# Kernel tuning notes

Hardware: AMD Instinct MI355X
Metric: run time of the kernel (lower is better)

Reference implementation:

```python
import jax, jax.numpy as jnp
import numpy as np

EMBED_DIM = 256; NUM_HEADS = 8; NUM_LEVELS = 4; NUM_POINTS = 4; FFN_DIM = 1024
SHAPES = [(128, 128), (64, 64), (32, 32), (16, 16)]
LN_EPS = 1e-5


def setup_inputs() -> dict:
    key = jax.random.key(0)
    ks = jax.random.split(key, 12)
    B = 2; C = EMBED_DIM
    Lin = sum(h * w for h, w in SHAPES)
    starts = np.concatenate([[0], np.cumsum([h * w for h, w in SHAPES])[:-1]])
    MLP2 = NUM_HEADS * NUM_LEVELS * NUM_POINTS
    p = lambda k, *s: jax.random.normal(k, s, jnp.float32) * 0.05
    return {
        "src": jax.random.normal(ks[0], (B, Lin, C), jnp.float32),
        "pos": jax.random.normal(ks[1], (B, Lin, C), jnp.float32),
        "reference_points": jax.random.uniform(ks[2], (B, Lin, NUM_LEVELS, 2), jnp.float32),
        "Wv": p(ks[3], C, C), "bv": jnp.zeros((C,), jnp.float32),
        "Wo": p(ks[4], C, MLP2 * 2),
        "bo": jax.random.uniform(ks[5], (MLP2 * 2,), jnp.float32, -2.0, 2.0),
        "Wa": p(ks[6], C, MLP2), "ba": jnp.zeros((MLP2,), jnp.float32),
        "Wout": p(ks[7], C, C), "bout": jnp.zeros((C,), jnp.float32),
        "gamma": jnp.ones((C,), jnp.float32), "beta": jnp.zeros((C,), jnp.float32),
        "W1": p(ks[8], C, FFN_DIM), "b1": jnp.zeros((FFN_DIM,), jnp.float32),
        "W2": p(ks[9], FFN_DIM, C), "b2": jnp.zeros((C,), jnp.float32),
        "spatial_shapes": jnp.array(SHAPES, dtype=jnp.int32),
        "level_start_index": jnp.array(starts, dtype=jnp.int32),
        "padding_mask": jnp.zeros((B, Lin), dtype=bool),
    }


def _layer_norm(x, g, b):
    m = jnp.mean(x, axis=-1, keepdims=True)
    v = jnp.mean((x - m) ** 2, axis=-1, keepdims=True)
    return (x - m) * jax.lax.rsqrt(v + LN_EPS) * g + b


def _bilinear_sample(val, loc, H, W):
    # val: [B, M, H*W, D]; loc: [B, M, Q, P, 2] normalized [0,1] (x, y)
    # matches torch grid_sample(align_corners=False, padding_mode='zeros')
    x = loc[..., 0] * W - 0.5
    y = loc[..., 1] * H - 0.5
    x0 = jnp.floor(x); y0 = jnp.floor(y)
    lx = x - x0; ly = y - y0
    x0 = x0.astype(jnp.int32); y0 = y0.astype(jnp.int32)
    Bm, M, Q, P = x0.shape
    out = jnp.zeros(val.shape[:2] + (Q, P, val.shape[-1]), val.dtype)
    corners = ((0, 0, (1 - lx) * (1 - ly)), (1, 0, lx * (1 - ly)),
               (0, 1, (1 - lx) * ly), (1, 1, lx * ly))
    for dx, dy, w in corners:
        xi = x0 + dx; yi = y0 + dy
        valid = (xi >= 0) & (xi < W) & (yi >= 0) & (yi < H)
        idx = jnp.clip(yi, 0, H - 1) * W + jnp.clip(xi, 0, W - 1)  # [B,M,Q,P]
        g = jnp.take_along_axis(val, idx.reshape(Bm, M, Q * P, 1), axis=2)
        g = g.reshape(Bm, M, Q, P, -1)
        out = out + (w * valid)[..., None] * g
    return out  # [B, M, Q, P, D]


def _forward(src, pos, reference_points, Wv, bv, Wo, bo, Wa, ba, Wout, bout,
             gamma, beta, W1, b1, W2, b2, spatial_shapes, level_start_index,
             padding_mask):
    M, L, P = NUM_HEADS, NUM_LEVELS, NUM_POINTS
    B, Lin, C = src.shape
    D = C // M
    shapes = np.asarray(spatial_shapes)          # static level geometry
    starts = np.asarray(level_start_index)
    query = src + pos
    value = src @ Wv + bv
    value = jnp.where(padding_mask[..., None], 0.0, value)
    value = value.reshape(B, Lin, M, D).transpose(0, 2, 1, 3)  # [B,M,Lin,D]
    Lq = query.shape[1]
    off = (query @ Wo + bo).reshape(B, Lq, M, L, P, 2)
    attn = jax.nn.softmax((query @ Wa + ba).reshape(B, Lq, M, L * P), axis=-1)
    attn = attn.reshape(B, Lq, M, L, P).transpose(0, 2, 1, 3, 4)  # [B,M,Lq,L,P]
    # offset normalizer is (W, H) per level
    normalizer = jnp.stack([spatial_shapes[:, 1], spatial_shapes[:, 0]], -1).astype(src.dtype)
    loc = reference_points[:, :, None, :, None, :] + off / normalizer[None, None, None, :, None, :]
    loc = loc.transpose(0, 2, 1, 3, 4, 5)  # [B,M,Lq,L,P,2]
    out = jnp.zeros((B, Lq, M, D), src.dtype)
    for l in range(L):
        H, W = int(shapes[l, 0]), int(shapes[l, 1])
        s = int(starts[l])
        vl = value[:, :, s:s + H * W, :]
        samp = _bilinear_sample(vl, loc[:, :, :, l], H, W)  # [B,M,Lq,P,D]
        out = out + jnp.einsum('bmqp,bmqpd->bqmd', attn[:, :, :, l], samp)
    src2 = out.reshape(B, Lq, C) @ Wout + bout
    x = _layer_norm(src + src2, gamma, beta)   # residual + norm (dropout is eval identity)
    h = jax.nn.relu(x @ W1 + b1)               # Mlp, no second residual in this module
    return h @ W2 + b2


def reference(src, pos, reference_points, Wv, bv, Wo, bo, Wa, ba, Wout, bout,
              gamma, beta, W1, b1, W2, b2, spatial_shapes, level_start_index,
              padding_mask):
    return _forward(src, pos, reference_points, Wv, bv, Wo, bo, Wa, ba, Wout,
                    bout, gamma, beta, W1, b1, W2, b2, spatial_shapes,
                    level_start_index, padding_mask)
```

## Files before the change

kernel.cpp:

```cpp
#include <hip/hip_runtime.h>
#include <hip/hip_bf16.h>
#include <math.h>

#define B_SZ   2
#define LIN    21760
#define C_DIM  256
#define M_H    8
#define D_H    32
#define NLEV   4
#define NPTS   4
#define FFN    1024
#define NTOK   (B_SZ * LIN)
#define LN_EPS 1e-5f

typedef __bf16 bf16;
typedef bf16  bf16x4 __attribute__((ext_vector_type(4)));
typedef bf16  bf16x8 __attribute__((ext_vector_type(8)));
typedef float f32x4  __attribute__((ext_vector_type(4)));

__device__ __constant__ int c_Ht[4] = {128, 64, 32, 16};
__device__ __constant__ int c_Wt[4] = {128, 64, 32, 16};
__device__ __constant__ int c_St[4] = {0, 16384, 20480, 21504};

static __device__ __forceinline__ float bf2f(unsigned short u) {
    union { float f; unsigned int i; } c;
    c.i = ((unsigned int)u) << 16;
    return c.f;
}

__global__ __launch_bounds__(256) void k_conv(const float* __restrict__ src,
                                              const float* __restrict__ pos,
                                              bf16* __restrict__ srcb,
                                              bf16* __restrict__ qb) {
    const int i = blockIdx.x * 256 + threadIdx.x;
    const float4 s4 = ((const float4*)src)[i];
    const float4 p4 = ((const float4*)pos)[i];
    bf16x4 sb, qb4;
    sb.x = (bf16)s4.x; sb.y = (bf16)s4.y; sb.z = (bf16)s4.z; sb.w = (bf16)s4.w;
    qb4.x = (bf16)(s4.x + p4.x); qb4.y = (bf16)(s4.y + p4.y);
    qb4.z = (bf16)(s4.z + p4.z); qb4.w = (bf16)(s4.w + p4.w);
    ((bf16x4*)srcb)[i] = sb;
    ((bf16x4*)qb)[i]   = qb4;
}

__global__ __launch_bounds__(256) void k_wt(const float* __restrict__ W,
                                            bf16* __restrict__ Wt,
                                            int K, int N, int nTilesN) {
    __shared__ float tile[32][33];
    const int bx = blockIdx.x % nTilesN;
    const int by = blockIdx.x / nTilesN;
    const int tx = threadIdx.x & 31, ty = threadIdx.x >> 5;
    const int n0 = bx * 32, k0 = by * 32;
#pragma unroll
    for (int i = 0; i < 32; i += 8)
        tile[ty + i][tx] = W[(long)(k0 + ty + i) * N + n0 + tx];
    __syncthreads();
#pragma unroll
    for (int i = 0; i < 32; i += 8)
        Wt[(long)(n0 + ty + i) * K + k0 + tx] = (bf16)tile[tx][ty + i];
}

#define GEMM_PROLOG(Aptr)                                                     \
    const int t = threadIdx.x;                                                \
    const int lane = t & 63, w = t >> 6;                                      \
    const int c0 = lane & 15, kg = lane >> 4;                                 \
    const long tok0 = (long)blockIdx.x * 32;                                  \
    {                                                                         \
        const bf16x8* src8 = (const bf16x8*)((Aptr) + tok0 * C_DIM);          \
        bf16x8* dst8 = (bf16x8*)xs;                                           \
        for (int i = t; i < 1024; i += 256)                                   \
            dst8[i ^ ((i >> 5) & 7)] = src8[i];                               \
    }                                                                         \
    __syncthreads();                                                          \
    bf16x8 afr[2][8];                                                         \
    _Pragma("unroll")                                                         \
    for (int mh = 0; mh < 2; ++mh) {                                          \
        const int m = mh * 16 + c0;                                           \
        _Pragma("unroll")                                                     \
        for (int kc = 0; kc < 8; ++kc) {                                      \
            const int chunk = m * 32 + kc * 4 + kg;                           \
            afr[mh][kc] = ((const bf16x8*)xs)[chunk ^ (m & 7)];               \
        }                                                                     \
    }

__global__ __launch_bounds__(256) void k_value_mfma(const bf16* __restrict__ A,
                                                    const bf16* __restrict__ Bw,
                                                    const float* __restrict__ bv,
                                                    bf16* __restrict__ value) {
    __shared__ bf16 xs[32 * 256];
    GEMM_PROLOG(A)

    const int b = (int)(tok0 / LIN);
    const int qbase = (int)(tok0 - (long)b * LIN);

#pragma unroll
    for (int nt = 0; nt < 4; ++nt) {
        const int n = w * 64 + nt * 16 + c0;
        f32x4 a0 = {0.f, 0.f, 0.f, 0.f};
        f32x4 a1 = {0.f, 0.f, 0.f, 0.f};
        const bf16* wrow = Bw + (long)n * 256 + kg * 8;
#pragma unroll
        for (int kc = 0; kc < 8; ++kc) {
            const bf16x8 bfr = *(const bf16x8*)(wrow + kc * 32);
            a0 = __builtin_amdgcn_mfma_f32_16x16x32_bf16(afr[0][kc], bfr, a0, 0, 0, 0);
            a1 = __builtin_amdgcn_mfma_f32_16x16x32_bf16(afr[1][kc], bfr, a1, 0, 0, 0);
        }
        const float bb = bv[n];
        const int m = n >> 5, d = n & 31;
        bf16* vb = value + ((long)(b * M_H + m) * LIN) * D_H + d;
#pragma unroll
        for (int r = 0; r < 4; ++r) {
            const int q0 = qbase + kg * 4 + r;
            vb[(long)q0 * D_H]        = (bf16)(a0[r] + bb);
            vb[(long)(q0 + 16) * D_H] = (bf16)(a1[r] + bb);
        }
    }
}

__global__ __launch_bounds__(256) void k_qloc_mfma(const bf16* __restrict__ A,
                                                   const bf16* __restrict__ Bw,
                                                   const float* __restrict__ bo,
                                                   const float* __restrict__ ba,
                                                   const float* __restrict__ refp,
                                                   float* __restrict__ loc,
                                                   float* __restrict__ att) {
    __shared__ bf16 xs[32 * 256];
    GEMM_PROLOG(A)

#pragma unroll
    for (int nt = 0; nt < 6; ++nt) {
        const int n = w * 96 + nt * 16 + c0;
        f32x4 a0 = {0.f, 0.f, 0.f, 0.f};
        f32x4 a1 = {0.f, 0.f, 0.f, 0.f};
        const bf16* wrow = Bw + (long)n * 256 + kg * 8;
#pragma unroll
        for (int kc = 0; kc < 8; ++kc) {
            const bf16x8 bfr = *(const bf16x8*)(wrow + kc * 32);
            a0 = __builtin_amdgcn_mfma_f32_16x16x32_bf16(afr[0][kc], bfr, a0, 0, 0, 0);
            a1 = __builtin_amdgcn_mfma_f32_16x16x32_bf16(afr[1][kc], bfr, a1, 0, 0, 0);
        }
        if (n < 256) {
            const int l = (n >> 3) & 3;
            const int c = n & 1;
            const float rnorm = 1.f / ((c == 0) ? (float)c_Wt[l] : (float)c_Ht[l]);
            const float bb = bo[n];
#pragma unroll
            for (int r = 0; r < 4; ++r) {
                const long t0 = tok0 + kg * 4 + r;
                const long t1 = t0 + 16;
                loc[t0 * C_DIM + n] = refp[t0 * 8 + l * 2 + c] + (a0[r] + bb) * rnorm;
                loc[t1 * C_DIM + n] = refp[t1 * 8 + l * 2 + c] + (a1[r] + bb) * rnorm;
            }
        } else {
            const int j = n - 256;
            const float bb = ba[j];
#pragma unroll
            for (int r = 0; r < 4; ++r) {
                const long t0 = tok0 + kg * 4 + r;
                att[t0 * 128 + j]        = a0[r] + bb;
                att[(t0 + 16) * 128 + j] = a1[r] + bb;
            }
        }
    }
}

__global__ __launch_bounds__(256) void k_samp(const unsigned short* __restrict__ value,
                                              const float* __restrict__ loc,
                                              const float* __restrict__ att,
                                              bf16* __restrict__ outb) {
    __shared__ int4   soff[128];
    __shared__ float4 swgt[128];
    const int t = threadIdx.x;
    const long tok = blockIdx.x;

    if (t < 128) {
        const float lg = att[tok * 128 + t];
        float mx = lg;
#pragma unroll
        for (int s = 1; s < 16; s <<= 1) mx = fmaxf(mx, __shfl_xor(mx, s));
        const float e = expf(lg - mx);
        float sm = e;
#pragma unroll
        for (int s = 1; s < 16; s <<= 1) sm += __shfl_xor(sm, s);
        const float a = e / sm;

        const float2 xy = ((const float2*)loc)[tok * 128 + t];
        const int l = (t >> 2) & 3;
        const int H = c_Ht[l], W = c_Wt[l], s0 = c_St[l];
        const float x = fmaf(xy.x, (float)W, -0.5f);
        const float y = fmaf(xy.y, (float)H, -0.5f);
        const float x0f = floorf(x), y0f = floorf(y);
        const float fx = x - x0f, fy = y - y0f;
        const int x0 = (int)x0f, y0 = (int)y0f;

        const int xi0 = min(max(x0, 0), W - 1);
        const int xi1 = min(max(x0 + 1, 0), W - 1);
        const int yi0 = min(max(y0, 0), H - 1);
        const int yi1 = min(max(y0 + 1, 0), H - 1);
        const float mx0 = (x0 >= 0 && x0 < W) ? 1.f : 0.f;
        const float mx1 = (x0 + 1 < W)        ? 1.f : 0.f;
        const float my0 = (y0 >= 0 && y0 < H) ? 1.f : 0.f;
        const float my1 = (y0 + 1 < H)        ? 1.f : 0.f;
        const float gx0 = (1.f - fx) * mx0, gx1 = fx * ((x0 + 1 >= 0) ? mx1 : 0.f);
        const float gy0 = (1.f - fy) * my0, gy1 = fy * ((y0 + 1 >= 0) ? my1 : 0.f);

        const int r0 = (s0 + yi0 * W) * D_H;
        const int r1 = (s0 + yi1 * W) * D_H;
        soff[t] = (int4){r0 + xi0 * D_H, r0 + xi1 * D_H, r1 + xi0 * D_H, r1 + xi1 * D_H};
        swgt[t] = (float4){a * gx0 * gy0, a * gx1 * gy0, a * gx0 * gy1, a * gx1 * gy1};
    }
    __syncthreads();

    const int m = t >> 5, d = t & 31;
    const int b = (int)(tok / LIN);
    const unsigned short* vb = value + ((long)(b * M_H + m)) * LIN * D_H + d;

    float acc = 0.f;
#pragma unroll
    for (int p = 0; p < 16; ++p) {
        const int jj = m * 16 + p;
        const int4   o = soff[jj];
        const float4 wv = swgt[jj];
        acc = fmaf(bf2f(vb[o.x]), wv.x, acc);
        acc = fmaf(bf2f(vb[o.y]), wv.y, acc);
        acc = fmaf(bf2f(vb[o.z]), wv.z, acc);
        acc = fmaf(bf2f(vb[o.w]), wv.w, acc);
    }
    outb[tok * C_DIM + t] = (bf16)acc;
}

__global__ __launch_bounds__(256) void k_post_mfma(const bf16* __restrict__ A,
                                                   const bf16* __restrict__ Bw,
                                                   const float* __restrict__ bout,
                                                   const float* __restrict__ src,
                                                   const float* __restrict__ g_,
                                                   const float* __restrict__ be_,
                                                   bf16* __restrict__ xb) {
    __shared__ bf16 xs[32 * 256];
    __shared__ float yt[32][256];
    GEMM_PROLOG(A)

#pragma unroll
    for (int nt = 0; nt < 4; ++nt) {
        const int n = w * 64 + nt * 16 + c0;
        f32x4 a0 = {0.f, 0.f, 0.f, 0.f};
        f32x4 a1 = {0.f, 0.f, 0.f, 0.f};
        const bf16* wrow = Bw + (long)n * 256 + kg * 8;
#pragma unroll
        for (int kc = 0; kc < 8; ++kc) {
            const bf16x8 bfr = *(const bf16x8*)(wrow + kc * 32);
            a0 = __builtin_amdgcn_mfma_f32_16x16x32_bf16(afr[0][kc], bfr, a0, 0, 0, 0);
            a1 = __builtin_amdgcn_mfma_f32_16x16x32_bf16(afr[1][kc], bfr, a1, 0, 0, 0);
        }
        const float bb = bout[n];
#pragma unroll
        for (int r = 0; r < 4; ++r) {
            const int row = kg * 4 + r;
            yt[row][n]      = a0[r] + bb + src[(tok0 + row) * C_DIM + n];
            yt[row + 16][n] = a1[r] + bb + src[(tok0 + row + 16) * C_DIM + n];
        }
    }
    __syncthreads();

    const float4 g4 = ((const float4*)g_)[lane];
    const float4 b4 = ((const float4*)be_)[lane];
#pragma unroll
    for (int rr = 0; rr < 8; ++rr) {
        const int row = w * 8 + rr;
        const float4 y4 = *(const float4*)&yt[row][lane * 4];
        float s1 = y4.x + y4.y + y4.z + y4.w;
        float s2 = y4.x * y4.x + y4.y * y4.y + y4.z * y4.z + y4.w * y4.w;
#pragma unroll
        for (int s = 1; s < 64; s <<= 1) {
            s1 += __shfl_xor(s1, s);
            s2 += __shfl_xor(s2, s);
        }
        const float mean = s1 * (1.f / 256.f);
        const float var  = s2 * (1.f / 256.f) - mean * mean;
        const float inv  = rsqrtf(var + LN_EPS);
        bf16x4 o;
        o.x = (bf16)((y4.x - mean) * inv * g4.x + b4.x);
        o.y = (bf16)((y4.y - mean) * inv * g4.y + b4.y);
        o.z = (bf16)((y4.z - mean) * inv * g4.z + b4.z);
        o.w = (bf16)((y4.w - mean) * inv * g4.w + b4.w);
        *(bf16x4*)(xb + (tok0 + row) * C_DIM + lane * 4) = o;
    }
}

__global__ __launch_bounds__(256) void k_ffn1(const bf16* __restrict__ x,
                                              const bf16* __restrict__ W1t,
                                              const float* __restrict__ b1,
                                              bf16* __restrict__ h) {
    const int t = threadIdx.x;
    const int lane = t & 63, w = t >> 6;
    const int c0 = lane & 15, kg = lane >> 4;
    const long tok0 = (long)blockIdx.x * 32;

    bf16x8 afr[2][8];
#pragma unroll
    for (int mh = 0; mh < 2; ++mh) {
        const long row = tok0 + mh * 16 + c0;
#pragma unroll
        for (int kc = 0; kc < 8; ++kc)
            afr[mh][kc] = *(const bf16x8*)(x + row * C_DIM + kc * 32 + kg * 8);
    }

    for (int nt = 0; nt < 16; ++nt) {
        const int n = w * 256 + nt * 16 + c0;
        f32x4 a0 = {0.f, 0.f, 0.f, 0.f};
        f32x4 a1 = {0.f, 0.f, 0.f, 0.f};
        const bf16* wrow = W1t + (long)n * 256 + kg * 8;
#pragma unroll
        for (int kc = 0; kc < 8; ++kc) {
            const bf16x8 bfr = *(const bf16x8*)(wrow + kc * 32);
            a0 = __builtin_amdgcn_mfma_f32_16x16x32_bf16(afr[0][kc], bfr, a0, 0, 0, 0);
            a1 = __builtin_amdgcn_mfma_f32_16x16x32_bf16(afr[1][kc], bfr, a1, 0, 0, 0);
        }
        const float bb = b1[n];
        bf16* hp = h + (tok0 + kg * 4) * FFN + n;
#pragma unroll
        for (int r = 0; r < 4; ++r) {
            hp[(long)r * FFN]        = (bf16)fmaxf(a0[r] + bb, 0.f);
            hp[(long)(r + 16) * FFN] = (bf16)fmaxf(a1[r] + bb, 0.f);
        }
    }
}

__global__ __launch_bounds__(256) void k_ffn2(const bf16* __restrict__ h,
                                              const bf16* __restrict__ W2t,
                                              const float* __restrict__ b2,
                                              float* __restrict__ out) {
    const int t = threadIdx.x;
    const int lane = t & 63, w = t >> 6;
    const int c0 = lane & 15, kg = lane >> 4;
    const long tok0 = (long)blockIdx.x * 32;

    f32x4 acc[2][4];
#pragma unroll
    for (int mh = 0; mh < 2; ++mh)
#pragma unroll
        for (int nt = 0; nt < 4; ++nt)
            acc[mh][nt] = (f32x4){0.f, 0.f, 0.f, 0.f};

    const bf16* ha = h + (tok0 + c0) * FFN + kg * 8;
    const bf16* hb = ha + 16 * FFN;
    for (int kc = 0; kc < 32; ++kc) {
        const int kb = kc * 32;
        const bf16x8 a0 = *(const bf16x8*)(ha + kb);
        const bf16x8 a1 = *(const bf16x8*)(hb + kb);
#pragma unroll
        for (int nt = 0; nt < 4; ++nt) {
            const int n = w * 64 + nt * 16 + c0;
            const bf16x8 bfr = *(const bf16x8*)(W2t + (long)n * FFN + kb + kg * 8);
            acc[0][nt] = __builtin_amdgcn_mfma_f32_16x16x32_bf16(a0, bfr, acc[0][nt], 0, 0, 0);
            acc[1][nt] = __builtin_amdgcn_mfma_f32_16x16x32_bf16(a1, bfr, acc[1][nt], 0, 0, 0);
        }
    }

#pragma unroll
    for (int nt = 0; nt < 4; ++nt) {
        const int n = w * 64 + nt * 16 + c0;
        const float bb = b2[n];
#pragma unroll
        for (int r = 0; r < 4; ++r) {
            out[(tok0 + kg * 4 + r) * C_DIM + n]      = acc[0][nt][r] + bb;
            out[(tok0 + 16 + kg * 4 + r) * C_DIM + n] = acc[1][nt][r] + bb;
        }
    }
}

extern "C" void kernel_launch(void* const* d_in, const int* in_sizes, int n_in,
                              void* d_out, int out_size, void* d_ws, size_t ws_size,
                              hipStream_t stream) {
    const float* src   = (const float*)d_in[0];
    const float* pos   = (const float*)d_in[1];
    const float* refp  = (const float*)d_in[2];
    const float* Wv    = (const float*)d_in[3];
    const float* bv    = (const float*)d_in[4];
    const float* Wo    = (const float*)d_in[5];
    const float* bo    = (const float*)d_in[6];
    const float* Wa    = (const float*)d_in[7];
    const float* ba    = (const float*)d_in[8];
    const float* Wout  = (const float*)d_in[9];
    const float* bout  = (const float*)d_in[10];
    const float* gamma = (const float*)d_in[11];
    const float* beta  = (const float*)d_in[12];
    const float* W1    = (const float*)d_in[13];
    const float* b1    = (const float*)d_in[14];
    const float* W2    = (const float*)d_in[15];
    const float* b2    = (const float*)d_in[16];

    const size_t N256 = (size_t)NTOK * C_DIM;
    bf16*  srcb = (bf16*)d_ws;
    bf16*  qb   = srcb + N256;
    bf16*  val  = qb + N256;
    float* loc  = (float*)(val + N256);
    float* att  = loc + N256;
    bf16*  Wvt  = (bf16*)(att + (size_t)NTOK * 128);
    bf16*  Wqt  = Wvt + 256 * 256;
    bf16*  Woutt= Wqt + 384 * 256;
    bf16*  W1t  = Woutt + 256 * 256;
    bf16*  W2t  = W1t + (size_t)FFN * C_DIM;
    bf16*  outb = srcb;
    bf16*  xb   = qb;
    bf16*  hbuf = val;

    dim3 blk(256);
    k_conv<<<NTOK * C_DIM / 4 / 256, blk, 0, stream>>>(src, pos, srcb, qb);
    k_wt<<<64,  blk, 0, stream>>>(Wv,   Wvt,           C_DIM, C_DIM, 8);
    k_wt<<<64,  blk, 0, stream>>>(Wo,   Wqt,           C_DIM, C_DIM, 8);
    k_wt<<<32,  blk, 0, stream>>>(Wa,   Wqt + 256*256, C_DIM, 128,   4);
    k_wt<<<64,  blk, 0, stream>>>(Wout, Woutt,         C_DIM, C_DIM, 8);
    k_wt<<<256, blk, 0, stream>>>(W1,   W1t,           C_DIM, FFN,   32);
    k_wt<<<256, blk, 0, stream>>>(W2,   W2t,           FFN,   C_DIM, 8);

    k_value_mfma<<<NTOK / 32, blk, 0, stream>>>(srcb, Wvt, bv, val);
    k_qloc_mfma <<<NTOK / 32, blk, 0, stream>>>(qb, Wqt, bo, ba, refp, loc, att);
    k_samp      <<<NTOK,      blk, 0, stream>>>((const unsigned short*)val, loc, att, outb);
    k_post_mfma <<<NTOK / 32, blk, 0, stream>>>(outb, Woutt, bout, src, gamma, beta, xb);
    k_ffn1      <<<NTOK / 32, blk, 0, stream>>>(xb, W1t, b1, hbuf);
    k_ffn2      <<<NTOK / 32, blk, 0, stream>>>(hbuf, W2t, b2, (float*)d_out);
}
```

Measured before the change: 496.5 us.

## Fuse FFN1 and FFN2 into one kernel with hidden chunk kept in LDS

Merges the two FFN GEMM kernels into a single kernel. Each block computes 256-wide chunks of the ReLU hidden activations into swizzled shared memory and immediately accumulates them into the second GEMM. This avoids writing and reading the bf16 hidden tensor (NTOK x 1024) through global memory and saves one launch. In exchange it adds block barriers and 32KB of LDS per block, which may lower occupancy. It also relies on a GEMM_PROLOG macro that is assumed to exist already.

```diff
diff --git a/kernel.cpp b/kernel.cpp
--- a/kernel.cpp
+++ b/kernel.cpp
@@ -287,53 +287,15 @@
     }
 }
 
-__global__ __launch_bounds__(256) void k_ffn1(const bf16* __restrict__ x,
-                                              const bf16* __restrict__ W1t,
-                                              const float* __restrict__ b1,
-                                              bf16* __restrict__ h) {
-    const int t = threadIdx.x;
-    const int lane = t & 63, w = t >> 6;
-    const int c0 = lane & 15, kg = lane >> 4;
-    const long tok0 = (long)blockIdx.x * 32;
-
-    bf16x8 afr[2][8];
-#pragma unroll
-    for (int mh = 0; mh < 2; ++mh) {
-        const long row = tok0 + mh * 16 + c0;
-#pragma unroll
-        for (int kc = 0; kc < 8; ++kc)
-            afr[mh][kc] = *(const bf16x8*)(x + row * C_DIM + kc * 32 + kg * 8);
-    }
-
-    for (int nt = 0; nt < 16; ++nt) {
-        const int n = w * 256 + nt * 16 + c0;
-        f32x4 a0 = {0.f, 0.f, 0.f, 0.f};
-        f32x4 a1 = {0.f, 0.f, 0.f, 0.f};
-        const bf16* wrow = W1t + (long)n * 256 + kg * 8;
-#pragma unroll
-        for (int kc = 0; kc < 8; ++kc) {
-            const bf16x8 bfr = *(const bf16x8*)(wrow + kc * 32);
-            a0 = __builtin_amdgcn_mfma_f32_16x16x32_bf16(afr[0][kc], bfr, a0, 0, 0, 0);
-            a1 = __builtin_amdgcn_mfma_f32_16x16x32_bf16(afr[1][kc], bfr, a1, 0, 0, 0);
-        }
-        const float bb = b1[n];
-        bf16* hp = h + (tok0 + kg * 4) * FFN + n;
-#pragma unroll
-        for (int r = 0; r < 4; ++r) {
-            hp[(long)r * FFN]        = (bf16)fmaxf(a0[r] + bb, 0.f);
-            hp[(long)(r + 16) * FFN] = (bf16)fmaxf(a1[r] + bb, 0.f);
-        }
-    }
-}
-
-__global__ __launch_bounds__(256) void k_ffn2(const bf16* __restrict__ h,
-                                              const bf16* __restrict__ W2t,
-                                              const float* __restrict__ b2,
-                                              float* __restrict__ out) {
-    const int t = threadIdx.x;
-    const int lane = t & 63, w = t >> 6;
-    const int c0 = lane & 15, kg = lane >> 4;
-    const long tok0 = (long)blockIdx.x * 32;
+__global__ __launch_bounds__(256) void k_ffn_mfma(const bf16* __restrict__ x,
+                                                  const bf16* __restrict__ W1t,
+                                                  const float* __restrict__ b1,
+                                                  const bf16* __restrict__ W2t,
+                                                  const float* __restrict__ b2,
+                                                  float* __restrict__ out) {
+    __shared__ bf16 xs[32 * 256];
+    __shared__ bf16 hs[32 * 256];
+    GEMM_PROLOG(x)
 
     f32x4 acc[2][4];
 #pragma unroll
@@ -342,18 +304,44 @@
         for (int nt = 0; nt < 4; ++nt)
             acc[mh][nt] = (f32x4){0.f, 0.f, 0.f, 0.f};
 
-    const bf16* ha = h + (tok0 + c0) * FFN + kg * 8;
-    const bf16* hb = ha + 16 * FFN;
-    for (int kc = 0; kc < 32; ++kc) {
-        const int kb = kc * 32;
-        const bf16x8 a0 = *(const bf16x8*)(ha + kb);
-        const bf16x8 a1 = *(const bf16x8*)(hb + kb);
+    for (int c = 0; c < 4; ++c) {
+        if (c) __syncthreads();
+
 #pragma unroll
         for (int nt = 0; nt < 4; ++nt) {
-            const int n = w * 64 + nt * 16 + c0;
-            const bf16x8 bfr = *(const bf16x8*)(W2t + (long)n * FFN + kb + kg * 8);
-            acc[0][nt] = __builtin_amdgcn_mfma_f32_16x16x32_bf16(a0, bfr, acc[0][nt], 0, 0, 0);
-            acc[1][nt] = __builtin_amdgcn_mfma_f32_16x16x32_bf16(a1, bfr, acc[1][nt], 0, 0, 0);
+            const int nl = w * 64 + nt * 16 + c0;
+            const int n  = c * 256 + nl;
+            f32x4 a0 = {0.f, 0.f, 0.f, 0.f};
+            f32x4 a1 = {0.f, 0.f, 0.f, 0.f};
+            const bf16* wrow = W1t + (long)n * 256 + kg * 8;
+#pragma unroll
+            for (int kc = 0; kc < 8; ++kc) {
+                const bf16x8 bfr = *(const bf16x8*)(wrow + kc * 32);
+                a0 = __builtin_amdgcn_mfma_f32_16x16x32_bf16(afr[0][kc], bfr, a0, 0, 0, 0);
+                a1 = __builtin_amdgcn_mfma_f32_16x16x32_bf16(afr[1][kc], bfr, a1, 0, 0, 0);
+            }
+            const float bb = b1[n];
+#pragma unroll
+            for (int r = 0; r < 4; ++r) {
+                const int row0 = kg * 4 + r;
+                hs[(row0 * 256 + nl)        ^ ((row0 & 7) << 3)] = (bf16)fmaxf(a0[r] + bb, 0.f);
+                hs[((row0 + 16) * 256 + nl) ^ ((row0 & 7) << 3)] = (bf16)fmaxf(a1[r] + bb, 0.f);
+            }
+        }
+        __syncthreads();
+
+#pragma unroll
+        for (int kc2 = 0; kc2 < 8; ++kc2) {
+            const int kl = kc2 * 32 + kg * 8;
+            const bf16x8 a0 = *(const bf16x8*)&hs[(c0 * 256 + kl)        ^ ((c0 & 7) << 3)];
+            const bf16x8 a1 = *(const bf16x8*)&hs[((c0 + 16) * 256 + kl) ^ ((c0 & 7) << 3)];
+#pragma unroll
+            for (int nt = 0; nt < 4; ++nt) {
+                const int n = w * 64 + nt * 16 + c0;
+                const bf16x8 bfr = *(const bf16x8*)(W2t + (long)n * FFN + c * 256 + kl);
+                acc[0][nt] = __builtin_amdgcn_mfma_f32_16x16x32_bf16(a0, bfr, acc[0][nt], 0, 0, 0);
+                acc[1][nt] = __builtin_amdgcn_mfma_f32_16x16x32_bf16(a1, bfr, acc[1][nt], 0, 0, 0);
+            }
         }
     }
 
@@ -403,7 +391,6 @@
     bf16*  W2t  = W1t + (size_t)FFN * C_DIM;
     bf16*  outb = srcb;
     bf16*  xb   = qb;
-    bf16*  hbuf = val;
 
     dim3 blk(256);
     k_conv<<<NTOK * C_DIM / 4 / 256, blk, 0, stream>>>(src, pos, srcb, qb);
@@ -418,6 +405,5 @@
     k_qloc_mfma <<<NTOK / 32, blk, 0, stream>>>(qb, Wqt, bo, ba, refp, loc, att);
     k_samp      <<<NTOK,      blk, 0, stream>>>((const unsigned short*)val, loc, att, outb);
     k_post_mfma <<<NTOK / 32, blk, 0, stream>>>(outb, Woutt, bout, src, gamma, beta, xb);
-    k_ffn1      <<<NTOK / 32, blk, 0, stream>>>(xb, W1t, b1, hbuf);
-    k_ffn2      <<<NTOK / 32, blk, 0, stream>>>(hbuf, W2t, b2, (float*)d_out);
-}
+    k_ffn_mfma  <<<NTOK / 32, blk, 0, stream>>>(xb, W1t, b1, W2t, b2, (float*)d_out);
+}
```

New measurement: 438.7 us. 1.13x faster.
